# Performance work log

Hardware: AMD Instinct MI355X
Metric: run time of the kernel (lower is better)

The kernel has to match this reference:

```python
import jax, jax.numpy as jnp
import numpy as np

N_NODES = 10000


def setup_inputs() -> dict:
    key = jax.random.key(0)
    k1, k2, k3 = jax.random.split(key, 3)
    x = jax.random.normal(k1, (N_NODES, 768), dtype=jnp.float32)
    edge_index = jax.random.randint(k2, (2, 100000), 0, N_NODES, dtype=jnp.int32)
    # GCNConv linear weight, stored [in, out] for x @ W
    W = jax.random.normal(k3, (768, 768), dtype=jnp.float32) * (1.0 / np.sqrt(768))
    b = jnp.zeros((768,), dtype=jnp.float32)
    return {"x": x, "edge_index": edge_index, "W": W, "b": b}


def reference(x, edge_index, W, b):
    # PyG GCNConv: add self-loops, symmetric degree normalization,
    # linear transform, then scatter-add aggregation (source -> target).
    n = x.shape[0]
    loops = jnp.arange(n, dtype=edge_index.dtype)
    row = jnp.concatenate([edge_index[0], loops])  # source nodes  [E+N]
    col = jnp.concatenate([edge_index[1], loops])  # target nodes  [E+N]

    ones = jnp.ones(row.shape[0], dtype=x.dtype)
    deg = jax.ops.segment_sum(ones, col, num_segments=n)          # in-degree incl. self-loop
    dinv = jnp.where(deg > 0, jax.lax.rsqrt(deg), 0.0)
    norm = dinv[row] * dinv[col]                                   # [E+N]

    h = x @ W                                                      # [N, out]
    msg = h[row] * norm[:, None]                                   # gather + scale
    out = jax.ops.segment_sum(msg, col, num_segments=n) + b        # scatter-add
    return out
```

## Files before the change

kernel.cpp:

```cpp
#include <hip/hip_runtime.h>
#include <hip/hip_bf16.h>
#include <stdint.h>

#define DIM 768
#define BM 128
#define BN 128
#define BK 64
#define SMAX 64

typedef __attribute__((ext_vector_type(8))) short short8;
typedef __attribute__((ext_vector_type(4))) float f32x4;

__device__ __forceinline__ void gload_lds16(const void* g, void* l) {
  __builtin_amdgcn_global_load_lds(
      (const __attribute__((address_space(1))) void*)g,
      (__attribute__((address_space(3))) void*)l, 16, 0, 0);
}

__device__ __forceinline__ unsigned short f2bf(float f) {
  union { __hip_bfloat16 h; unsigned short u; } cv;
  cv.h = __float2bfloat16(f);
  return cv.u;
}

__device__ __forceinline__ float bf2f(unsigned short u) {
  return __uint_as_float(((unsigned)u) << 16);
}


#define WT_TILES 576
#define CVTX_BLOCKS 3750

__global__ __launch_bounds__(256) void prep_kernel(
    const float* __restrict__ x, const float* __restrict__ W,
    unsigned short* __restrict__ xbf, unsigned short* __restrict__ wt,
    const int* __restrict__ row, const int* __restrict__ col, int E,
    int* __restrict__ cnt, int* __restrict__ srcs, int N) {
  __shared__ float tile[32][33];
  const int b = blockIdx.x;
  const int t = threadIdx.x;
  if (b < WT_TILES) {
    int bx = b % (DIM / 32), by = b / (DIM / 32);
    int n0 = bx * 32, k0 = by * 32;
    int tx = t & 31, ty = t >> 5;
#pragma unroll
    for (int i = 0; i < 4; ++i) {
      int r = ty + i * 8;
      tile[r][tx] = W[(size_t)(k0 + r) * DIM + n0 + tx];
    }
    __syncthreads();
#pragma unroll
    for (int i = 0; i < 4; ++i) {
      int r = ty + i * 8;
      wt[(size_t)(n0 + r) * DIM + k0 + tx] = f2bf(tile[tx][r]);
    }
  } else if (b < WT_TILES + CVTX_BLOCKS) {
    int i = (b - WT_TILES) * 256 + t;
    if (i < N * DIM / 8) {
      const float4* xp = ((const float4*)x) + (size_t)i * 2;
      float4 v0 = xp[0], v1 = xp[1];
      ushort4 o0, o1;
      o0.x = f2bf(v0.x); o0.y = f2bf(v0.y); o0.z = f2bf(v0.z); o0.w = f2bf(v0.w);
      o1.x = f2bf(v1.x); o1.y = f2bf(v1.y); o1.z = f2bf(v1.z); o1.w = f2bf(v1.w);
      ushort4* op = ((ushort4*)xbf) + (size_t)i * 2;
      op[0] = o0; op[1] = o1;
    }
  } else {
    int i = (b - WT_TILES - CVTX_BLOCKS) * 256 + t;
    if (i < E) {
      int c = col[i];
      int pos = atomicAdd(&cnt[c], 1);
      if (pos < SMAX) srcs[c * SMAX + pos] = row[i];
    }
  }
}


__global__ __launch_bounds__(256) void gemm_kernel(
    const unsigned short* __restrict__ xbf, const unsigned short* __restrict__ wt,
    const int* __restrict__ cnt, unsigned short* __restrict__ g, int M) {
  __shared__ __align__(16) unsigned short Als[BM * BK];
  __shared__ __align__(16) unsigned short Bls[BN * BK];
  const int t = threadIdx.x;
  const int gemmBlocks = gridDim.x;

  int fid = blockIdx.x;
  int q = gemmBlocks >> 3, r8 = gemmBlocks & 7;
  int xcd = fid & 7, ii = fid >> 3;
  int nid = (xcd < r8 ? xcd * (q + 1) : r8 * (q + 1) + (xcd - r8) * q) + ii;
  const int tile_m = (nid / (DIM / BN)) * BM;
  const int n0 = (nid % (DIM / BN)) * BN;

  const int lane = t & 63;
  const int w = t >> 6;
  const int wr = w >> 1, wc = w & 1;

  f32x4 acc[4][4];
#pragma unroll
  for (int i = 0; i < 4; ++i)
#pragma unroll
    for (int j = 0; j < 4; ++j) acc[i][j] = (f32x4){0.f, 0.f, 0.f, 0.f};

  for (int kt = 0; kt < DIM / BK; ++kt) {
    const int k0 = kt * BK;
    __syncthreads();
#pragma unroll
    for (int it = 0; it < 4; ++it) {
      int p = it * 256 + t;
      int r = p >> 3;
      int gl = (p & 7) ^ (r & 7);
      int ga = tile_m + r;
      if (ga > M - 1) ga = M - 1;
      gload_lds16(xbf + (size_t)ga * DIM + k0 + gl * 8, (char*)Als + p * 16);
      gload_lds16(wt + (size_t)(n0 + r) * DIM + k0 + gl * 8, (char*)Bls + p * 16);
    }
    __syncthreads();

#pragma unroll
    for (int kk = 0; kk < 2; ++kk) {
      short8 a[4], b[4];
#pragma unroll
      for (int mi = 0; mi < 4; ++mi) {
        int r = wr * 64 + mi * 16 + (lane & 15);
        int ch = kk * 4 + (lane >> 4);
        a[mi] = *(const short8*)((const char*)Als + r * 128 + ((ch ^ (r & 7)) * 16));
      }
#pragma unroll
      for (int ni = 0; ni < 4; ++ni) {
        int c = wc * 64 + ni * 16 + (lane & 15);
        int ch = kk * 4 + (lane >> 4);
        b[ni] = *(const short8*)((const char*)Bls + c * 128 + ((ch ^ (c & 7)) * 16));
      }
#pragma unroll
      for (int mi = 0; mi < 4; ++mi)
#pragma unroll
        for (int ni = 0; ni < 4; ++ni)
          acc[mi][ni] = __builtin_amdgcn_mfma_f32_16x16x32_bf16(a[mi], b[ni], acc[mi][ni], 0, 0, 0);
    }
  }

#pragma unroll
  for (int mi = 0; mi < 4; ++mi) {
#pragma unroll
    for (int reg = 0; reg < 4; ++reg) {
      int m = tile_m + wr * 64 + mi * 16 + (lane >> 4) * 4 + reg;
      if (m < M) {
        float dv = rsqrtf((float)cnt[m] + 1.0f);
#pragma unroll
        for (int ni = 0; ni < 4; ++ni) {
          int n = n0 + wc * 64 + ni * 16 + (lane & 15);
          g[(size_t)m * DIM + n] = f2bf(dv * acc[mi][ni][reg]);
        }
      }
    }
  }
}


__global__ __launch_bounds__(192) void agg_kernel(
    const unsigned short* __restrict__ g, const int* __restrict__ cnt,
    const int* __restrict__ srcs, const float* __restrict__ b,
    float* __restrict__ out) {
  __shared__ int sidx[SMAX];
  int c = blockIdx.x;
  int t = threadIdx.x;
  int deg = cnt[c];
  if (deg > SMAX) deg = SMAX;
  if (t < deg) sidx[t] = srcs[c * SMAX + t];
  const ushort4* gr = (const ushort4*)(g + (size_t)c * DIM);
  ushort4 v = gr[t];
  float a0 = bf2f(v.x), a1 = bf2f(v.y), a2 = bf2f(v.z), a3 = bf2f(v.w);
  __syncthreads();
  int j = 0;
  for (; j + 4 <= deg; j += 4) {
    int i0 = sidx[j], i1 = sidx[j + 1], i2 = sidx[j + 2], i3 = sidx[j + 3];
    ushort4 u0 = ((const ushort4*)(g + (size_t)i0 * DIM))[t];
    ushort4 u1 = ((const ushort4*)(g + (size_t)i1 * DIM))[t];
    ushort4 u2 = ((const ushort4*)(g + (size_t)i2 * DIM))[t];
    ushort4 u3 = ((const ushort4*)(g + (size_t)i3 * DIM))[t];
    a0 += bf2f(u0.x) + bf2f(u1.x) + bf2f(u2.x) + bf2f(u3.x);
    a1 += bf2f(u0.y) + bf2f(u1.y) + bf2f(u2.y) + bf2f(u3.y);
    a2 += bf2f(u0.z) + bf2f(u1.z) + bf2f(u2.z) + bf2f(u3.z);
    a3 += bf2f(u0.w) + bf2f(u1.w) + bf2f(u2.w) + bf2f(u3.w);
  }
  for (; j < deg; ++j) {
    ushort4 u = ((const ushort4*)(g + (size_t)sidx[j] * DIM))[t];
    a0 += bf2f(u.x); a1 += bf2f(u.y); a2 += bf2f(u.z); a3 += bf2f(u.w);
  }
  float dv = rsqrtf((float)deg + 1.0f);
  float4 bb = ((const float4*)b)[t];
  float4 r;
  r.x = dv * a0 + bb.x;
  r.y = dv * a1 + bb.y;
  r.z = dv * a2 + bb.z;
  r.w = dv * a3 + bb.w;
  ((float4*)(out + (size_t)c * DIM))[t] = r;
}


extern "C" void kernel_launch(void* const* d_in, const int* in_sizes, int n_in,
                              void* d_out, int out_size, void* d_ws, size_t ws_size,
                              hipStream_t stream) {
  const float* x = (const float*)d_in[0];
  const int* ei = (const int*)d_in[1];
  const float* W = (const float*)d_in[2];
  const float* b = (const float*)d_in[3];
  float* out = (float*)d_out;
  const int N = in_sizes[0] / DIM;
  const int E = in_sizes[1] / 2;
  const int* row = ei;
  const int* col = ei + E;

  char* ws = (char*)d_ws;
  size_t off = 0;
  auto alloc = [&](size_t bytes) {
    size_t o = off;
    off = (off + bytes + 15) & ~(size_t)15;
    return o;
  };
  int* cnt   = (int*)(ws + alloc((size_t)N * 4));
  int* srcs  = (int*)(ws + alloc((size_t)N * SMAX * 4));
  unsigned short* xbf = (unsigned short*)(ws + alloc((size_t)N * DIM * 2));
  unsigned short* wt  = (unsigned short*)(ws + alloc((size_t)DIM * DIM * 2));
  unsigned short* g   = (unsigned short*)(ws + alloc((size_t)N * DIM * 2));

  int fill_blocks = (E + 255) / 256;
  int gemm_blocks = ((N + BM - 1) / BM) * (DIM / BN);

  hipMemsetAsync(cnt, 0, (size_t)N * 4, stream);
  prep_kernel<<<WT_TILES + CVTX_BLOCKS + fill_blocks, 256, 0, stream>>>(
      x, W, xbf, wt, row, col, E, cnt, srcs, N);
  gemm_kernel<<<gemm_blocks, 256, 0, stream>>>(xbf, wt, cnt, g, N);
  agg_kernel<<<N, 192, 0, stream>>>(g, cnt, srcs, b, out);
}
```

Before: 75.71 us.

## Fold count zeroing into prep and run edge fill alongside GEMM

Removes the separate hipMemsetAsync by zeroing the degree counters inside the prep kernel. The CSR-style edge bucketing moves out of prep and into extra blocks of the GEMM launch, so the atomics can overlap with the matmul. Because degrees are no longer known when the GEMM epilogue runs, the source-side normalization moves to the aggregation kernel, which looks up each neighbor's degree and scales it per edge. This adds per-edge multiplies and an indirect cnt read in aggregation, and the fill blocks are launched after the GEMM blocks, so they may finish late and extend the GEMM kernel's tail.

```diff
diff --git a/kernel.cpp b/kernel.cpp
--- a/kernel.cpp
+++ b/kernel.cpp
@@ -7,6 +7,7 @@
 #define BN 128
 #define BK 64
 #define SMAX 64
+#define FILL_BLOCKS 64
 
 typedef __attribute__((ext_vector_type(8))) short short8;
 typedef __attribute__((ext_vector_type(4))) float f32x4;
@@ -34,8 +35,7 @@
 __global__ __launch_bounds__(256) void prep_kernel(
     const float* __restrict__ x, const float* __restrict__ W,
     unsigned short* __restrict__ xbf, unsigned short* __restrict__ wt,
-    const int* __restrict__ row, const int* __restrict__ col, int E,
-    int* __restrict__ cnt, int* __restrict__ srcs, int N) {
+    int* __restrict__ cnt, int N) {
   __shared__ float tile[32][33];
   const int b = blockIdx.x;
   const int t = threadIdx.x;
@@ -67,22 +67,33 @@
     }
   } else {
     int i = (b - WT_TILES - CVTX_BLOCKS) * 256 + t;
-    if (i < E) {
+#pragma unroll
+    for (int j = 0; j < 4; ++j) {
+      int idx = i * 4 + j;
+      if (idx < N) cnt[idx] = 0;
+    }
+  }
+}
+
+
+__global__ __launch_bounds__(256) void gemm_fill_kernel(
+    const unsigned short* __restrict__ xbf, const unsigned short* __restrict__ wt,
+    unsigned short* __restrict__ g, int M,
+    const int* __restrict__ row, const int* __restrict__ col, int E,
+    int* __restrict__ cnt, int* __restrict__ srcs, int gemmBlocks) {
+  __shared__ __align__(16) unsigned short Als[BM * BK];
+  __shared__ __align__(16) unsigned short Bls[BN * BK];
+  const int t = threadIdx.x;
+
+  if ((int)blockIdx.x >= gemmBlocks) {
+    int i0 = ((int)blockIdx.x - gemmBlocks) * 256 + t;
+    for (int i = i0; i < E; i += FILL_BLOCKS * 256) {
       int c = col[i];
       int pos = atomicAdd(&cnt[c], 1);
       if (pos < SMAX) srcs[c * SMAX + pos] = row[i];
     }
-  }
-}
-
-
-__global__ __launch_bounds__(256) void gemm_kernel(
-    const unsigned short* __restrict__ xbf, const unsigned short* __restrict__ wt,
-    const int* __restrict__ cnt, unsigned short* __restrict__ g, int M) {
-  __shared__ __align__(16) unsigned short Als[BM * BK];
-  __shared__ __align__(16) unsigned short Bls[BN * BK];
-  const int t = threadIdx.x;
-  const int gemmBlocks = gridDim.x;
+    return;
+  }
 
   int fid = blockIdx.x;
   int q = gemmBlocks >> 3, r8 = gemmBlocks & 7;
@@ -145,11 +156,10 @@
     for (int reg = 0; reg < 4; ++reg) {
       int m = tile_m + wr * 64 + mi * 16 + (lane >> 4) * 4 + reg;
       if (m < M) {
-        float dv = rsqrtf((float)cnt[m] + 1.0f);
 #pragma unroll
         for (int ni = 0; ni < 4; ++ni) {
           int n = n0 + wc * 64 + ni * 16 + (lane & 15);
-          g[(size_t)m * DIM + n] = f2bf(dv * acc[mi][ni][reg]);
+          g[(size_t)m * DIM + n] = f2bf(acc[mi][ni][reg]);
         }
       }
     }
@@ -162,32 +172,41 @@
     const int* __restrict__ srcs, const float* __restrict__ b,
     float* __restrict__ out) {
   __shared__ int sidx[SMAX];
+  __shared__ float sdsc[SMAX];
   int c = blockIdx.x;
   int t = threadIdx.x;
   int deg = cnt[c];
   if (deg > SMAX) deg = SMAX;
-  if (t < deg) sidx[t] = srcs[c * SMAX + t];
+  if (t < deg) {
+    int s = srcs[c * SMAX + t];
+    sidx[t] = s;
+    sdsc[t] = rsqrtf((float)cnt[s] + 1.0f);
+  }
+  float dv = rsqrtf((float)deg + 1.0f);
   const ushort4* gr = (const ushort4*)(g + (size_t)c * DIM);
   ushort4 v = gr[t];
-  float a0 = bf2f(v.x), a1 = bf2f(v.y), a2 = bf2f(v.z), a3 = bf2f(v.w);
+  float a0 = dv * bf2f(v.x), a1 = dv * bf2f(v.y);
+  float a2 = dv * bf2f(v.z), a3 = dv * bf2f(v.w);
   __syncthreads();
   int j = 0;
   for (; j + 4 <= deg; j += 4) {
     int i0 = sidx[j], i1 = sidx[j + 1], i2 = sidx[j + 2], i3 = sidx[j + 3];
+    float d0 = sdsc[j], d1 = sdsc[j + 1], d2 = sdsc[j + 2], d3 = sdsc[j + 3];
     ushort4 u0 = ((const ushort4*)(g + (size_t)i0 * DIM))[t];
     ushort4 u1 = ((const ushort4*)(g + (size_t)i1 * DIM))[t];
     ushort4 u2 = ((const ushort4*)(g + (size_t)i2 * DIM))[t];
     ushort4 u3 = ((const ushort4*)(g + (size_t)i3 * DIM))[t];
-    a0 += bf2f(u0.x) + bf2f(u1.x) + bf2f(u2.x) + bf2f(u3.x);
-    a1 += bf2f(u0.y) + bf2f(u1.y) + bf2f(u2.y) + bf2f(u3.y);
-    a2 += bf2f(u0.z) + bf2f(u1.z) + bf2f(u2.z) + bf2f(u3.z);
-    a3 += bf2f(u0.w) + bf2f(u1.w) + bf2f(u2.w) + bf2f(u3.w);
+    a0 += d0 * bf2f(u0.x) + d1 * bf2f(u1.x) + d2 * bf2f(u2.x) + d3 * bf2f(u3.x);
+    a1 += d0 * bf2f(u0.y) + d1 * bf2f(u1.y) + d2 * bf2f(u2.y) + d3 * bf2f(u3.y);
+    a2 += d0 * bf2f(u0.z) + d1 * bf2f(u1.z) + d2 * bf2f(u2.z) + d3 * bf2f(u3.z);
+    a3 += d0 * bf2f(u0.w) + d1 * bf2f(u1.w) + d2 * bf2f(u2.w) + d3 * bf2f(u3.w);
   }
   for (; j < deg; ++j) {
+    float dj = sdsc[j];
     ushort4 u = ((const ushort4*)(g + (size_t)sidx[j] * DIM))[t];
-    a0 += bf2f(u.x); a1 += bf2f(u.y); a2 += bf2f(u.z); a3 += bf2f(u.w);
-  }
-  float dv = rsqrtf((float)deg + 1.0f);
+    a0 += dj * bf2f(u.x); a1 += dj * bf2f(u.y);
+    a2 += dj * bf2f(u.z); a3 += dj * bf2f(u.w);
+  }
   float4 bb = ((const float4*)b)[t];
   float4 r;
   r.x = dv * a0 + bb.x;
@@ -224,12 +243,12 @@
   unsigned short* wt  = (unsigned short*)(ws + alloc((size_t)DIM * DIM * 2));
   unsigned short* g   = (unsigned short*)(ws + alloc((size_t)N * DIM * 2));
 
-  int fill_blocks = (E + 255) / 256;
+  int zero_blocks = (N + 1023) / 1024;
   int gemm_blocks = ((N + BM - 1) / BM) * (DIM / BN);
 
-  hipMemsetAsync(cnt, 0, (size_t)N * 4, stream);
-  prep_kernel<<<WT_TILES + CVTX_BLOCKS + fill_blocks, 256, 0, stream>>>(
-      x, W, xbf, wt, row, col, E, cnt, srcs, N);
-  gemm_kernel<<<gemm_blocks, 256, 0, stream>>>(xbf, wt, cnt, g, N);
+  prep_kernel<<<WT_TILES + CVTX_BLOCKS + zero_blocks, 256, 0, stream>>>(
+      x, W, xbf, wt, cnt, N);
+  gemm_fill_kernel<<<gemm_blocks + FILL_BLOCKS, 256, 0, stream>>>(
+      xbf, wt, g, N, row, col, E, cnt, srcs, gemm_blocks);
   agg_kernel<<<N, 192, 0, stream>>>(g, cnt, srcs, b, out);
 }
```

After: 63.71 us. 15.8% less time.
